# Performance work log

Measured on AMD Instinct MI355X. Metric: run time of the kernel, lower is better.

The kernel has to match this reference:

```python
import jax, jax.numpy as jnp
import numpy as np

FEATURE_STRIDE = 16
CFG = {"TRAIN": dict(pre=12000, post=2000, thresh=0.7, min_size=16.0),
       "TEST":  dict(pre=6000,  post=300,  thresh=0.7, min_size=16.0)}

def _generate_anchors(base_size=16, ratios=(0.5, 1.0, 2.0), scales=(8, 16, 32)):
    xc = yc = (base_size - 1) * 0.5
    size = float(base_size * base_size)
    out = []
    for r in ratios:
        w = np.round(np.sqrt(size / r))
        h = np.round(w * r)
        for s in scales:
            W, H = w * s, h * s
            out.append([xc - 0.5 * (W - 1), yc - 0.5 * (H - 1),
                        xc + 0.5 * (W - 1), yc + 0.5 * (H - 1)])
    return np.array(out, np.float32)

ANCHORS = jnp.asarray(_generate_anchors())  # (9, 4)
NUM_ANCHORS = ANCHORS.shape[0]

def _pairwise_iou(b):
    x1, y1, x2, y2 = b[:, 0], b[:, 1], b[:, 2], b[:, 3]
    area = (x2 - x1 + 1.0) * (y2 - y1 + 1.0)
    iw = jnp.clip(jnp.minimum(x2[:, None], x2[None]) - jnp.maximum(x1[:, None], x1[None]) + 1.0, 0.0)
    ih = jnp.clip(jnp.minimum(y2[:, None], y2[None]) - jnp.maximum(y1[:, None], y1[None]) + 1.0, 0.0)
    inter = iw * ih
    return inter / (area[:, None] + area[None] - inter)

def _nms_keep(boxes, valid, thresh):
    # greedy NMS over score-sorted boxes; returns bool keep mask
    K = boxes.shape[0]
    iou = _pairwise_iou(boxes)  # (K, K)
    rng = jnp.arange(K)
    def body(i, keep):
        conflict = jnp.any((rng < i) & keep & (iou[i] > thresh))
        return keep.at[i].set(valid[i] & ~conflict)
    return jax.lax.fori_loop(0, K, body, jnp.zeros((K,), bool))

def reference(rpn_cls_scores, rpn_bbox_adjusts, img_shapes, train):
    cfg = CFG["TRAIN" if train else "TEST"]
    B, _, H, W = rpn_cls_scores.shape
    A = NUM_ANCHORS
    # fg scores: channels [A:2A], layout (h, w, a) after permute
    scores = rpn_cls_scores[:, A:].transpose(0, 2, 3, 1).reshape(B, -1)      # (B, N)
    deltas = rpn_bbox_adjusts.transpose(0, 2, 3, 1).reshape(B, -1, 4)        # (B, N, 4)
    # all anchors on the feature grid
    sx = jnp.arange(W, dtype=jnp.float32) * FEATURE_STRIDE
    sy = jnp.arange(H, dtype=jnp.float32) * FEATURE_STRIDE
    gy, gx = jnp.meshgrid(sy, sx, indexing="ij")
    shifts = jnp.stack([gx, gy, gx, gy], -1).reshape(-1, 4)                  # (H*W, 4)
    anchors = (shifts[:, None, :] + ANCHORS[None]).reshape(-1, 4)            # (N, 4)
    # bbox_transform_inv (+1 convention)
    aw = anchors[:, 2] - anchors[:, 0] + 1.0
    ah = anchors[:, 3] - anchors[:, 1] + 1.0
    acx = anchors[:, 0] + 0.5 * aw
    acy = anchors[:, 1] + 0.5 * ah
    pcx = deltas[..., 0] * aw + acx
    pcy = deltas[..., 1] * ah + acy
    pw = jnp.exp(deltas[..., 2]) * aw
    ph = jnp.exp(deltas[..., 3]) * ah
    x1, y1 = pcx - 0.5 * pw, pcy - 0.5 * ph
    x2, y2 = pcx + 0.5 * pw, pcy + 0.5 * ph
    imh, imw = img_shapes[:, 0:1], img_shapes[:, 1:2]
    x1 = jnp.clip(x1, 0.0, imw - 1.0); x2 = jnp.clip(x2, 0.0, imw - 1.0)
    y1 = jnp.clip(y1, 0.0, imh - 1.0); y2 = jnp.clip(y2, 0.0, imh - 1.0)
    boxes = jnp.stack([x1, y1, x2, y2], -1)                                  # (B, N, 4)
    valid = ((x2 - x1 + 1.0) >= cfg["min_size"]) & ((y2 - y1 + 1.0) >= cfg["min_size"])
    masked = jnp.where(valid, scores, -jnp.inf)
    K = min(cfg["pre"], boxes.shape[1])
    top_s, idx = jax.lax.top_k(masked, K)                                    # (B, K)
    top_b = jnp.take_along_axis(boxes, idx[..., None], axis=1)               # (B, K, 4)
    keep = jax.vmap(lambda b, v: _nms_keep(b, v, cfg["thresh"]))(
        jax.lax.stop_gradient(top_b), jnp.isfinite(top_s))
    post = cfg["post"]
    fin_s = jnp.where(keep, top_s, -jnp.inf)
    sel_s, idx2 = jax.lax.top_k(fin_s, post)
    sel_b = jnp.take_along_axis(top_b, idx2[..., None], axis=1)              # (B, post, 4)
    sel_b = jnp.where(jnp.isfinite(sel_s)[..., None], sel_b, 0.0)
    bix = jnp.broadcast_to(jnp.arange(B, dtype=sel_b.dtype)[:, None, None], (B, post, 1))
    return jnp.concatenate([bix, sel_b], -1)                                 # (B, post, 5)

def setup_inputs():
    key = jax.random.key(0)
    k1, k2 = jax.random.split(key)
    B, H, W = 4, 64, 96
    rpn_cls_scores = jax.random.normal(k1, (B, 2 * NUM_ANCHORS, H, W), jnp.float32)
    rpn_bbox_adjusts = jax.random.normal(k2, (B, 4 * NUM_ANCHORS, H, W), jnp.float32) * 0.1
    img_shapes = jnp.tile(jnp.array([[1024.0, 1536.0]], jnp.float32), (B, 1))
    return {"rpn_cls_scores": rpn_cls_scores, "rpn_bbox_adjusts": rpn_bbox_adjusts,
            "img_shapes": img_shapes, "train": 0}
```

## Files before the change

kernel.cpp:

```cpp
#include <hip/hip_runtime.h>


#define NB 4
#define AH 64
#define AW 96
#define NA 9
#define NPOS (AH*AW)
#define NPC (NPOS*NA)
#define LDSN 8192
#define HBITS 15
#define HSZ (1<<HBITS)
#define HSH (32-HBITS)
#define NTHR 1024
#define WIN 2048
#define DYN_LDS (65536 + 50560)

typedef unsigned long long u64;
typedef unsigned int u32;

__constant__ float c_anchors[NA][4] = {
  { -84.f,  -40.f,  99.f,  55.f},
  {-176.f,  -88.f, 191.f, 103.f},
  {-360.f, -184.f, 375.f, 199.f},
  { -56.f,  -56.f,  71.f,  71.f},
  {-120.f, -120.f, 135.f, 135.f},
  {-248.f, -248.f, 263.f, 263.f},
  { -36.f,  -80.f,  51.f,  95.f},
  { -80.f, -168.f,  95.f, 183.f},
  {-168.f, -344.f, 183.f, 359.f},
};

__device__ u32    g_keys[NB][NPC];
__device__ float4 g_boxes[NB][NPC];
__device__ u32    g_h15[NB][HSZ];
__device__ float4 g_sbox[NB][LDSN];

__device__ __forceinline__ bool iou_gt(float4 a, float areaA, float4 q, float areaQ) {
#pragma clang fp contract(off)
  float iw = fminf(a.z, q.z) - fmaxf(a.x, q.x) + 1.0f; iw = fmaxf(iw, 0.0f);
  float ih = fminf(a.w, q.w) - fmaxf(a.y, q.y) + 1.0f; ih = fmaxf(ih, 0.0f);
  float inter = iw * ih;
  float denom = areaA + areaQ - inter;
  float d = inter - 0.7f * denom;
  if (__builtin_expect(fabsf(d) <= 4e-6f * denom, 0))
    return (inter / denom) > 0.7f;
  return d > 0.0f;
}

__global__ void __launch_bounds__(256)
kA_decode(const float* __restrict__ cls, const float* __restrict__ dlt,
          const float* __restrict__ ish) {
#pragma clang fp contract(off)
  const int UPB = NPOS/256;
  int bid = blockIdx.x;
  int b   = bid / (NA*UPB);
  int r   = bid % (NA*UPB);
  int a   = r / UPB;
  int pos = (r % UPB) * 256 + threadIdx.x;
  int i2  = a * NPOS + pos;

  int wx = pos % AW;
  int hy = pos / AW;

  float score = cls[(b * (2*NA) + NA + a) * NPOS + pos];
  const float* dp = dlt + (b * (4*NA) + a*4) * NPOS + pos;
  float d0 = dp[0];
  float d1 = dp[NPOS];
  float d2 = dp[2*NPOS];
  float d3 = dp[3*NPOS];

  float shx = (float)(wx * 16);
  float shy = (float)(hy * 16);
  float ax1 = c_anchors[a][0] + shx;
  float ay1 = c_anchors[a][1] + shy;
  float ax2 = c_anchors[a][2] + shx;
  float ay2 = c_anchors[a][3] + shy;

  float aw_ = ax2 - ax1 + 1.0f;
  float ah_ = ay2 - ay1 + 1.0f;
  float acx = ax1 + 0.5f * aw_;
  float acy = ay1 + 0.5f * ah_;

  float pcx = d0 * aw_ + acx;
  float pcy = d1 * ah_ + acy;
  float pw  = expf(d2) * aw_;
  float ph  = expf(d3) * ah_;

  float x1 = pcx - 0.5f * pw;
  float y1 = pcy - 0.5f * ph;
  float x2 = pcx + 0.5f * pw;
  float y2 = pcy + 0.5f * ph;

  float imh = ish[b*2 + 0];
  float imw = ish[b*2 + 1];
  x1 = fminf(fmaxf(x1, 0.0f), imw - 1.0f);
  x2 = fminf(fmaxf(x2, 0.0f), imw - 1.0f);
  y1 = fminf(fmaxf(y1, 0.0f), imh - 1.0f);
  y2 = fminf(fmaxf(y2, 0.0f), imh - 1.0f);

  bool valid = ((x2 - x1 + 1.0f) >= 16.0f) && ((y2 - y1 + 1.0f) >= 16.0f);

  g_boxes[b][i2] = make_float4(x1, y1, x2, y2);

  u32 key = 0u;
  if (valid) {
    u32 ub = __float_as_uint(score);
    key = (ub >> 31) ? ~ub : (ub | 0x80000000u);
  }
  g_keys[b][i2] = key;
  atomicAdd(&g_h15[b][key >> HSH], 1u);
}

__global__ void __launch_bounds__(NTHR)
kB_sortnms(float* __restrict__ out, const int* __restrict__ train, int post) {
#pragma clang fp contract(off)
  const int tid = threadIdx.x;
  const int b   = blockIdx.x;
  const int pre = train[0] ? 12000 : 6000;
  const int lane = tid & 63;
  const int wid  = tid >> 6;

  extern __shared__ __align__(16) unsigned char smem[];
  u64* sl = (u64*)smem;
  unsigned char* r2 = smem + 65536;
  u32* base = (u32*)r2;
  u32* cntw = base + WIN;

  __shared__ u32 gsum[32];
  __shared__ u32 gsuf[33];
  __shared__ int sG;
  __shared__ int sT;
  __shared__ u32 sU0;
  __shared__ int s_nk;

  {
    int g = tid >> 5, j = tid & 31;
    const u32* __restrict__ hg = &g_h15[b][g * 1024];
    u32 part = 0;
#pragma unroll
    for (int k = 0; k < 32; ++k) part += hg[k*32 + j];
#pragma unroll
    for (int m = 16; m >= 1; m >>= 1) part += __shfl_xor(part, m);
    if (j == 0) gsum[g] = part;
  }
  if (tid == 0) { sG = -1; sT = -1; s_nk = 0; }
  __syncthreads();
  if (tid == 0) {
    u32 r = 0; gsuf[32] = 0;
    for (int g = 31; g >= 0; --g) { r += gsum[g]; gsuf[g] = r; }
  }
  __syncthreads();
  if (tid < 32 && gsuf[tid] >= (u32)pre) atomicMax(&sG, tid);
  __syncthreads();
  const int G  = sG;
  const int Gc = (G < 0) ? 0 : G;
  cntw[tid] = g_h15[b][Gc * 1024 + tid];
  __syncthreads();
  for (int d = 1; d < 1024; d <<= 1) {
    u32 add = (tid + d < 1024) ? cntw[tid + d] : 0u;
    __syncthreads();
    cntw[tid] += add;
    __syncthreads();
  }
  if (G >= 0) {
    u32 sfx = gsuf[G + 1] + cntw[tid];
    if (sfx >= (u32)pre && (G * 1024 + tid) >= 1) atomicMax(&sT, tid);
  }
  __syncthreads();
  int P; u32 SP;
  if (sT >= 0) { P = G * 1024 + sT; SP = gsuf[G + 1] + cntw[sT]; }
  else         { P = 1; SP = gsuf[0] - g_h15[b][0]; }
  const u32 pivot = (u32)P << HSH;
  const u32 hP = g_h15[b][P];
  __syncthreads();
  {
    int i0 = P + 1 + tid, i1 = i0 + 1024;
    base[tid]        = (i0 < HSZ) ? g_h15[b][i0] : 0u;
    base[tid + 1024] = (i1 < HSZ) ? g_h15[b][i1] : 0u;
  }
  __syncthreads();
  for (int d = 1; d < 2048; d <<= 1) {
    u32 a0 = (tid + d < 2048) ? base[tid + d] : 0u;
    u32 a1 = (tid + 1024 + d < 2048) ? base[tid + 1024 + d] : 0u;
    __syncthreads();
    base[tid] += a0;
    base[tid + 1024] += a1;
    __syncthreads();
  }
  if (tid == 0) sU0 = base[0];
  __syncthreads();
  {
    u32 adj = SP - hP - sU0;
    base[tid] += adj;
    base[tid + 1024] += adj;
    cntw[tid] = 0u;
    cntw[tid + 1024] = 0u;
  }
  __syncthreads();
  int C = (int)SP; if (C > LDSN) C = LDSN;
  const int Kb = min(pre, C);

  for (int i2 = tid; i2 < NPC; i2 += NTHR) {
    u32 key = g_keys[b][i2];
    if (key >= pivot) {
      int w = (int)(key >> HSH) - P;
      if (w < 0) w = 0; if (w > WIN-1) w = WIN-1;
      int slot = (int)base[w] + (int)atomicAdd(&cntw[w], 1u);
      if (slot < LDSN) {
        int a = i2 / NPOS, pos = i2 - a * NPOS;
        u32 iref = (u32)(pos * NA + a);
        sl[slot] = ((u64)key << 32) | (u64)(0xFFFFFFFFu - iref);
      }
    }
  }
  __syncthreads();

  for (int w = wid; w < WIN; w += 16) {
    int cw = (int)cntw[w];
    if (cw < 2) continue;
    int bse = (int)base[w];
    if (cw <= 64) {
      u64 v0 = (lane < cw) ? sl[bse + lane] : 0ull;
      for (int k = 2; k <= 64; k <<= 1) {
        for (int j = k >> 1; j; j >>= 1) {
          u64 o = __shfl_xor(v0, j);
          bool dir   = ((lane & k) == 0);
          bool lower = ((lane & j) == 0);
          v0 = ((v0 > o) == (lower == dir)) ? v0 : o;
        }
      }
      if (lane < cw) sl[bse + lane] = v0;
    } else {
      if (cw > 256) cw = 256;
      u64 v[4];
#pragma unroll
      for (int s = 0; s < 4; ++s) {
        int idx = s*64 + lane;
        v[s] = (idx < cw) ? sl[bse + idx] : 0ull;
      }
      for (int k = 2; k <= 256; k <<= 1) {
        for (int j = k >> 1; j; j >>= 1) {
          if (j >= 64) {
            int js = j >> 6;
#pragma unroll
            for (int sa = 0; sa < 4; ++sa) {
              int sb = sa ^ js;
              if (sb > sa) {
                int idx = sa*64 + lane;
                bool dir = ((idx & k) == 0);
                u64 A = v[sa], B = v[sb];
                if ((A < B) == dir) { v[sa] = B; v[sb] = A; }
              }
            }
          } else {
#pragma unroll
            for (int s = 0; s < 4; ++s) {
              u64 o = __shfl_xor(v[s], j);
              int idx = s*64 + lane;
              bool dir   = ((idx & k) == 0);
              bool lower = ((lane & j) == 0);
              v[s] = ((v[s] > o) == (lower == dir)) ? v[s] : o;
            }
          }
        }
      }
#pragma unroll
      for (int s = 0; s < 4; ++s) {
        int idx = s*64 + lane;
        if (idx < cw) sl[bse + idx] = v[s];
      }
    }
  }
  __syncthreads();

  for (int r = tid; r < Kb; r += NTHR) {
    u32 iref = 0xFFFFFFFFu - (u32)(sl[r] & 0xFFFFFFFFull);
    int pos = iref / NA, a = iref - pos * NA;
    g_sbox[b][r] = g_boxes[b][a * NPOS + pos];
  }
  __syncthreads();

  {
    float4* kbox = (float4*)r2;
    float*  kar  = (float*)(r2 + 32768);
    float4* cbox = (float4*)(r2 + 40960);
    float*  car  = (float*)(r2 + 41984);
    u64 (*conf16)[64] = (u64 (*)[64])(r2 + 42240);
    u64* sup16 = (u64*)(r2 + 50432);

    if (wid == 15) {
      float4 bx0 = (lane < Kb) ? g_sbox[b][lane] : make_float4(0.f,0.f,-1.f,-1.f);
      cbox[lane] = bx0;
      car[lane]  = (bx0.z - bx0.x + 1.0f) * (bx0.w - bx0.y + 1.0f);
    }
    __syncthreads();

    int nk = 0;
    u64 laneBitsBelow = (lane == 0) ? 0ull : (~0ull >> (64 - lane));

    for (int bs = 0; bs < Kb; bs += 64) {
      float4 bx  = cbox[lane];
      float area = car[lane];
      bool active = (bs + lane < Kb);

      float4 nxt = make_float4(0.f, 0.f, -1.f, -1.f);
      if (wid == 15) {
        int c2 = bs + 64 + lane;
        if (c2 < Kb) nxt = g_sbox[b][c2];
      }

      int supp = active ? 0 : 1;
      {
        int t = wid;
        for (; t + 48 < nk; t += 64) {
          supp |= (int)iou_gt(bx, area, kbox[t],    kar[t]);
          supp |= (int)iou_gt(bx, area, kbox[t+16], kar[t+16]);
          supp |= (int)iou_gt(bx, area, kbox[t+32], kar[t+32]);
          supp |= (int)iou_gt(bx, area, kbox[t+48], kar[t+48]);
        }
        for (; t < nk; t += 16) supp |= (int)iou_gt(bx, area, kbox[t], kar[t]);
      }
      u64 sb = __ballot(supp);
      if (lane == 0) sup16[wid] = sb;

      {
        u64 confp = 0ull;
#pragma unroll
        for (int q = 0; q < 4; ++q) {
          int j = (wid << 2) + q;
          if (iou_gt(bx, area, cbox[j], car[j])) confp |= (1ull << j);
        }
        conf16[wid][lane] = confp;
      }
      __syncthreads();

      if (wid == 0) {
        u64 conf = 0ull;
#pragma unroll
        for (int w = 0; w < 16; ++w) conf |= conf16[w][lane];
        conf &= laneBitsBelow;
        u64 supAll = 0ull;
#pragma unroll
        for (int w = 0; w < 16; ++w) supAll |= sup16[w];
        u64 pending = ~supAll;
        u64 keptmask = 0ull;
        while (pending) {
          int i = __ffsll(pending) - 1;
          keptmask |= (1ull << i);
          u64 confb = __ballot((int)((conf >> i) & 1ull));
          pending &= ~confb;
          pending &= ~(1ull << i);
        }
        int myPos = nk + __popcll(keptmask & laneBitsBelow);
        if (((keptmask >> lane) & 1ull) && myPos < post) {
          kbox[myPos] = bx;
          kar [myPos] = area;
          float* o = out + ((size_t)b * post + myPos) * 5;
          o[0] = (float)b; o[1] = bx.x; o[2] = bx.y; o[3] = bx.z; o[4] = bx.w;
        }
        if (lane == 0) s_nk = nk + __popcll(keptmask);
      } else if (wid == 15) {
        cbox[lane] = nxt;
        car[lane]  = (nxt.z - nxt.x + 1.0f) * (nxt.w - nxt.y + 1.0f);
      }
      __syncthreads();
      nk = s_nk;
      if (nk >= post) break;
    }

    nk = min(nk, post);
    for (int rr = nk + tid; rr < post; rr += NTHR) {
      float* o = out + ((size_t)b * post + rr) * 5;
      o[0] = (float)b; o[1] = 0.0f; o[2] = 0.0f; o[3] = 0.0f; o[4] = 0.0f;
    }
  }

  {
    uint4* hz = (uint4*)&g_h15[b][0];
    uint4 z = make_uint4(0u,0u,0u,0u);
    for (int q = tid; q < HSZ/4; q += NTHR) hz[q] = z;
  }
}

extern "C" void kernel_launch(void* const* d_in, const int* in_sizes, int n_in,
                              void* d_out, int out_size, void* d_ws, size_t ws_size,
                              hipStream_t stream) {
  (void)in_sizes; (void)n_in; (void)d_ws; (void)ws_size;
  const float* cls   = (const float*)d_in[0];
  const float* dlt   = (const float*)d_in[1];
  const float* ish   = (const float*)d_in[2];
  const int*   train = (const int*)d_in[3];
  float* out = (float*)d_out;

  int post = out_size / (NB * 5);

  (void)hipFuncSetAttribute((const void*)kB_sortnms,
      hipFuncAttributeMaxDynamicSharedMemorySize, DYN_LDS);

  kA_decode<<<NB*NA*(NPOS/256), 256, 0, stream>>>(cls, dlt, ish);
  kB_sortnms<<<NB, NTHR, DYN_LDS, stream>>>(out, train, post);
}
```

Baseline: 192.8 us.

## Split sort and NMS into separate kernels and use wave-shuffle scans

```diff
diff --git a/kernel.cpp b/kernel.cpp
--- a/kernel.cpp
+++ b/kernel.cpp
@@ -13,7 +13,7 @@
 #define HSH (32-HBITS)
 #define NTHR 1024
 #define WIN 2048
-#define DYN_LDS (65536 + 50560)
+#define DYN_B1 (65536 + WIN*4*2)
 
 typedef unsigned long long u64;
 typedef unsigned int u32;
@@ -34,6 +34,7 @@
 __device__ float4 g_boxes[NB][NPC];
 __device__ u32    g_h15[NB][HSZ];
 __device__ float4 g_sbox[NB][LDSN];
+__device__ int    g_kb[NB];
 
 __device__ __forceinline__ bool iou_gt(float4 a, float areaA, float4 q, float areaQ) {
 #pragma clang fp contract(off)
@@ -112,8 +113,7 @@
 }
 
 __global__ void __launch_bounds__(NTHR)
-kB_sortnms(float* __restrict__ out, const int* __restrict__ train, int post) {
-#pragma clang fp contract(off)
+kB1_sort(const int* __restrict__ train) {
   const int tid = threadIdx.x;
   const int b   = blockIdx.x;
   const int pre = train[0] ? 12000 : 6000;
@@ -121,17 +121,18 @@
   const int wid  = tid >> 6;
 
   extern __shared__ __align__(16) unsigned char smem[];
-  u64* sl = (u64*)smem;
-  unsigned char* r2 = smem + 65536;
-  u32* base = (u32*)r2;
+  u64* sl   = (u64*)smem;
+  u32* base = (u32*)(smem + 65536);
   u32* cntw = base + WIN;
 
   __shared__ u32 gsum[32];
   __shared__ u32 gsuf[33];
+  __shared__ u32 wtot[16];
   __shared__ int sG;
   __shared__ int sT;
-  __shared__ u32 sU0;
-  __shared__ int s_nk;
+  __shared__ u32 sSP;
+
+  if (tid == 0) { sG = -1; sT = -1; sSP = 0u; }
 
   {
     int g = tid >> 5, j = tid & 31;
@@ -143,62 +144,85 @@
     for (int m = 16; m >= 1; m >>= 1) part += __shfl_xor(part, m);
     if (j == 0) gsum[g] = part;
   }
-  if (tid == 0) { sG = -1; sT = -1; s_nk = 0; }
-  __syncthreads();
-  if (tid == 0) {
-    u32 r = 0; gsuf[32] = 0;
-    for (int g = 31; g >= 0; --g) { r += gsum[g]; gsuf[g] = r; }
-  }
-  __syncthreads();
-  if (tid < 32 && gsuf[tid] >= (u32)pre) atomicMax(&sG, tid);
-  __syncthreads();
+  __syncthreads();
+
+  if (tid < 32) {
+    u32 v = gsum[tid];
+#pragma unroll
+    for (int m = 1; m < 32; m <<= 1) {
+      u32 t = __shfl_down(v, m);
+      if (tid + m < 32) v += t;
+    }
+    gsuf[tid] = v;
+    if (tid == 0) gsuf[32] = 0u;
+  }
+  __syncthreads();
+
+  if (tid < 32 && gsuf[tid] >= (u32)pre &&
+      (tid == 31 || gsuf[tid+1] < (u32)pre)) sG = tid;
+  __syncthreads();
+
   const int G  = sG;
   const int Gc = (G < 0) ? 0 : G;
-  cntw[tid] = g_h15[b][Gc * 1024 + tid];
-  __syncthreads();
-  for (int d = 1; d < 1024; d <<= 1) {
-    u32 add = (tid + d < 1024) ? cntw[tid + d] : 0u;
-    __syncthreads();
-    cntw[tid] += add;
-    __syncthreads();
-  }
-  if (G >= 0) {
-    u32 sfx = gsuf[G + 1] + cntw[tid];
-    if (sfx >= (u32)pre && (G * 1024 + tid) >= 1) atomicMax(&sT, tid);
-  }
-  __syncthreads();
+
+  u32 hv = g_h15[b][Gc*1024 + (wid<<6) + lane];
+  u32 sfx = hv;
+#pragma unroll
+  for (int m = 1; m < 64; m <<= 1) {
+    u32 t = __shfl_down(sfx, m);
+    if (lane + m < 64) sfx += t;
+  }
+  if (lane == 0) wtot[wid] = sfx;
+  __syncthreads();
+  {
+    u32 wsuf = 0;
+    for (int w2 = wid + 1; w2 < 16; ++w2) wsuf += wtot[w2];
+    u32 sfxg = __shfl(sfx, 0) - ( __shfl(sfx,0) - sfx );
+    sfxg = sfx + wsuf;
+    if (G >= 0) {
+      int t = (wid<<6) + lane;
+      u32 S = gsuf[G+1] + sfxg;
+      bool c0 = (S >= (u32)pre);
+      bool c1 = (t < 1023) && ((S - hv) >= (u32)pre);
+      if (c0 && !c1) {
+        int bin = Gc*1024 + t;
+        if (bin >= 1) { sT = t; sSP = S; }
+      }
+    }
+  }
+  __syncthreads();
+
   int P; u32 SP;
-  if (sT >= 0) { P = G * 1024 + sT; SP = gsuf[G + 1] + cntw[sT]; }
+  if (sT >= 0) { P = Gc*1024 + sT; SP = sSP; }
   else         { P = 1; SP = gsuf[0] - g_h15[b][0]; }
   const u32 pivot = (u32)P << HSH;
-  const u32 hP = g_h15[b][P];
-  __syncthreads();
+
   {
-    int i0 = P + 1 + tid, i1 = i0 + 1024;
-    base[tid]        = (i0 < HSZ) ? g_h15[b][i0] : 0u;
-    base[tid + 1024] = (i1 < HSZ) ? g_h15[b][i1] : 0u;
-  }
-  __syncthreads();
-  for (int d = 1; d < 2048; d <<= 1) {
-    u32 a0 = (tid + d < 2048) ? base[tid + d] : 0u;
-    u32 a1 = (tid + 1024 + d < 2048) ? base[tid + 1024 + d] : 0u;
+    int b0 = P + (wid<<7) + (lane<<1);
+    u32 h0 = (b0 < HSZ) ? g_h15[b][b0] : 0u;
+    u32 h1 = (b0+1 < HSZ) ? g_h15[b][b0+1] : 0u;
+    u32 pfx = h0 + h1;
+#pragma unroll
+    for (int m = 1; m < 64; m <<= 1) {
+      u32 t = __shfl_up(pfx, m);
+      if (lane >= m) pfx += t;
+    }
+    if (lane == 63) wtot[wid] = pfx;
     __syncthreads();
-    base[tid] += a0;
-    base[tid + 1024] += a1;
-    __syncthreads();
-  }
-  if (tid == 0) sU0 = base[0];
-  __syncthreads();
-  {
-    u32 adj = SP - hP - sU0;
-    base[tid] += adj;
-    base[tid + 1024] += adj;
-    cntw[tid] = 0u;
-    cntw[tid + 1024] = 0u;
-  }
-  __syncthreads();
+    u32 woff = 0;
+    for (int w2 = 0; w2 < wid; ++w2) woff += wtot[w2];
+    u32 pc1 = woff + pfx;
+    u32 pc0 = pc1 - h1;
+    int w0 = (wid<<7) + (lane<<1);
+    base[w0]   = SP - pc0;
+    base[w0+1] = SP - pc1;
+    cntw[w0] = 0u; cntw[w0+1] = 0u;
+  }
+  __syncthreads();
+
   int C = (int)SP; if (C > LDSN) C = LDSN;
   const int Kb = min(pre, C);
+  if (tid == 0) g_kb[b] = Kb;
 
   for (int i2 = tid; i2 < NPC; i2 += NTHR) {
     u32 key = g_keys[b][i2];
@@ -278,107 +302,117 @@
     int pos = iref / NA, a = iref - pos * NA;
     g_sbox[b][r] = g_boxes[b][a * NPOS + pos];
   }
-  __syncthreads();
-
-  {
-    float4* kbox = (float4*)r2;
-    float*  kar  = (float*)(r2 + 32768);
-    float4* cbox = (float4*)(r2 + 40960);
-    float*  car  = (float*)(r2 + 41984);
-    u64 (*conf16)[64] = (u64 (*)[64])(r2 + 42240);
-    u64* sup16 = (u64*)(r2 + 50432);
-
-    if (wid == 15) {
-      float4 bx0 = (lane < Kb) ? g_sbox[b][lane] : make_float4(0.f,0.f,-1.f,-1.f);
-      cbox[lane] = bx0;
-      car[lane]  = (bx0.z - bx0.x + 1.0f) * (bx0.w - bx0.y + 1.0f);
-    }
-    __syncthreads();
-
-    int nk = 0;
-    u64 laneBitsBelow = (lane == 0) ? 0ull : (~0ull >> (64 - lane));
-
-    for (int bs = 0; bs < Kb; bs += 64) {
-      float4 bx  = cbox[lane];
-      float area = car[lane];
-      bool active = (bs + lane < Kb);
-
-      float4 nxt = make_float4(0.f, 0.f, -1.f, -1.f);
-      if (wid == 15) {
-        int c2 = bs + 64 + lane;
-        if (c2 < Kb) nxt = g_sbox[b][c2];
-      }
-
-      int supp = active ? 0 : 1;
-      {
-        int t = wid;
-        for (; t + 48 < nk; t += 64) {
-          supp |= (int)iou_gt(bx, area, kbox[t],    kar[t]);
-          supp |= (int)iou_gt(bx, area, kbox[t+16], kar[t+16]);
-          supp |= (int)iou_gt(bx, area, kbox[t+32], kar[t+32]);
-          supp |= (int)iou_gt(bx, area, kbox[t+48], kar[t+48]);
-        }
-        for (; t < nk; t += 16) supp |= (int)iou_gt(bx, area, kbox[t], kar[t]);
-      }
-      u64 sb = __ballot(supp);
-      if (lane == 0) sup16[wid] = sb;
-
-      {
-        u64 confp = 0ull;
-#pragma unroll
-        for (int q = 0; q < 4; ++q) {
-          int j = (wid << 2) + q;
-          if (iou_gt(bx, area, cbox[j], car[j])) confp |= (1ull << j);
-        }
-        conf16[wid][lane] = confp;
-      }
-      __syncthreads();
-
-      if (wid == 0) {
-        u64 conf = 0ull;
-#pragma unroll
-        for (int w = 0; w < 16; ++w) conf |= conf16[w][lane];
-        conf &= laneBitsBelow;
-        u64 supAll = 0ull;
-#pragma unroll
-        for (int w = 0; w < 16; ++w) supAll |= sup16[w];
-        u64 pending = ~supAll;
-        u64 keptmask = 0ull;
-        while (pending) {
-          int i = __ffsll(pending) - 1;
-          keptmask |= (1ull << i);
-          u64 confb = __ballot((int)((conf >> i) & 1ull));
-          pending &= ~confb;
-          pending &= ~(1ull << i);
-        }
-        int myPos = nk + __popcll(keptmask & laneBitsBelow);
-        if (((keptmask >> lane) & 1ull) && myPos < post) {
-          kbox[myPos] = bx;
-          kar [myPos] = area;
-          float* o = out + ((size_t)b * post + myPos) * 5;
-          o[0] = (float)b; o[1] = bx.x; o[2] = bx.y; o[3] = bx.z; o[4] = bx.w;
-        }
-        if (lane == 0) s_nk = nk + __popcll(keptmask);
-      } else if (wid == 15) {
-        cbox[lane] = nxt;
-        car[lane]  = (nxt.z - nxt.x + 1.0f) * (nxt.w - nxt.y + 1.0f);
-      }
-      __syncthreads();
-      nk = s_nk;
-      if (nk >= post) break;
-    }
-
-    nk = min(nk, post);
-    for (int rr = nk + tid; rr < post; rr += NTHR) {
-      float* o = out + ((size_t)b * post + rr) * 5;
-      o[0] = (float)b; o[1] = 0.0f; o[2] = 0.0f; o[3] = 0.0f; o[4] = 0.0f;
-    }
-  }
 
   {
     uint4* hz = (uint4*)&g_h15[b][0];
     uint4 z = make_uint4(0u,0u,0u,0u);
     for (int q = tid; q < HSZ/4; q += NTHR) hz[q] = z;
+  }
+}
+
+__global__ void __launch_bounds__(NTHR)
+kC_nms(float* __restrict__ out, int post) {
+#pragma clang fp contract(off)
+  const int tid = threadIdx.x;
+  const int b   = blockIdx.x;
+  const int lane = tid & 63;
+  const int wid  = tid >> 6;
+
+  __shared__ float4 kbox[2048];
+  __shared__ float  kar [2048];
+  __shared__ float4 cbox[64];
+  __shared__ float  car [64];
+  __shared__ u64 conf16[16][64];
+  __shared__ u64 sup16[16];
+  __shared__ int s_nk;
+
+  const int Kb = g_kb[b];
+  if (tid == 0) s_nk = 0;
+
+  if (wid == 15) {
+    float4 bx0 = (lane < Kb) ? g_sbox[b][lane] : make_float4(0.f,0.f,-1.f,-1.f);
+    cbox[lane] = bx0;
+    car[lane]  = (bx0.z - bx0.x + 1.0f) * (bx0.w - bx0.y + 1.0f);
+  }
+  __syncthreads();
+
+  int nk = 0;
+  u64 laneBitsBelow = (lane == 0) ? 0ull : (~0ull >> (64 - lane));
+
+  for (int bs = 0; bs < Kb; bs += 64) {
+    float4 bx  = cbox[lane];
+    float area = car[lane];
+    bool active = (bs + lane < Kb);
+
+    float4 nxt = make_float4(0.f, 0.f, -1.f, -1.f);
+    if (wid == 15) {
+      int c2 = bs + 64 + lane;
+      if (c2 < Kb) nxt = g_sbox[b][c2];
+    }
+
+    int supp = active ? 0 : 1;
+    {
+      int t = wid;
+      for (; t + 48 < nk; t += 64) {
+        supp |= (int)iou_gt(bx, area, kbox[t],    kar[t]);
+        supp |= (int)iou_gt(bx, area, kbox[t+16], kar[t+16]);
+        supp |= (int)iou_gt(bx, area, kbox[t+32], kar[t+32]);
+        supp |= (int)iou_gt(bx, area, kbox[t+48], kar[t+48]);
+      }
+      for (; t < nk; t += 16) supp |= (int)iou_gt(bx, area, kbox[t], kar[t]);
+    }
+    u64 sb = __ballot(supp);
+    if (lane == 0) sup16[wid] = sb;
+
+    {
+      u64 confp = 0ull;
+#pragma unroll
+      for (int q = 0; q < 4; ++q) {
+        int j = (wid << 2) + q;
+        if (iou_gt(bx, area, cbox[j], car[j])) confp |= (1ull << j);
+      }
+      conf16[wid][lane] = confp;
+    }
+    __syncthreads();
+
+    if (wid == 0) {
+      u64 conf = 0ull;
+#pragma unroll
+      for (int w = 0; w < 16; ++w) conf |= conf16[w][lane];
+      conf &= laneBitsBelow;
+      u64 supAll = 0ull;
+#pragma unroll
+      for (int w = 0; w < 16; ++w) supAll |= sup16[w];
+      u64 pending = ~supAll;
+      u64 keptmask = 0ull;
+      while (pending) {
+        int i = __ffsll(pending) - 1;
+        keptmask |= (1ull << i);
+        u64 confb = __ballot((int)((conf >> i) & 1ull));
+        pending &= ~confb;
+        pending &= ~(1ull << i);
+      }
+      int myPos = nk + __popcll(keptmask & laneBitsBelow);
+      if (((keptmask >> lane) & 1ull) && myPos < post) {
+        kbox[myPos] = bx;
+        kar [myPos] = area;
+        float* o = out + ((size_t)b * post + myPos) * 5;
+        o[0] = (float)b; o[1] = bx.x; o[2] = bx.y; o[3] = bx.z; o[4] = bx.w;
+      }
+      if (lane == 0) s_nk = nk + __popcll(keptmask);
+    } else if (wid == 15) {
+      cbox[lane] = nxt;
+      car[lane]  = (nxt.z - nxt.x + 1.0f) * (nxt.w - nxt.y + 1.0f);
+    }
+    __syncthreads();
+    nk = s_nk;
+    if (nk >= post) break;
+  }
+
+  nk = min(nk, post);
+  for (int rr = nk + tid; rr < post; rr += NTHR) {
+    float* o = out + ((size_t)b * post + rr) * 5;
+    o[0] = (float)b; o[1] = 0.0f; o[2] = 0.0f; o[3] = 0.0f; o[4] = 0.0f;
   }
 }
 
@@ -394,9 +428,10 @@
 
   int post = out_size / (NB * 5);
 
-  (void)hipFuncSetAttribute((const void*)kB_sortnms,
-      hipFuncAttributeMaxDynamicSharedMemorySize, DYN_LDS);
+  (void)hipFuncSetAttribute((const void*)kB1_sort,
+      hipFuncAttributeMaxDynamicSharedMemorySize, DYN_B1);
 
   kA_decode<<<NB*NA*(NPOS/256), 256, 0, stream>>>(cls, dlt, ish);
-  kB_sortnms<<<NB, NTHR, DYN_LDS, stream>>>(out, train, post);
+  kB1_sort<<<NB, NTHR, DYN_B1, stream>>>(train);
+  kC_nms<<<NB, NTHR, 0, stream>>>(out, post);
 }
```

Result: no change. 190.5 us (-1.2%).
